# Performance work log

Measured on AMD Instinct MI355X. Metric: run time of the kernel, lower is better.

The kernel has to match this reference:

```python
import jax, jax.numpy as jnp
import numpy as np

D_MODEL = 1024
N_HEAD = 16
HEAD_DIM = D_MODEL // N_HEAD  # 64
B, T = 2, 2048
ROPE_BASE = 10000.0


def _rotary_cos_sin(seq_len, head_dim, dtype):
    inv_freq = 1.0 / (ROPE_BASE ** (jnp.arange(0, head_dim, 2, dtype=jnp.float32) / head_dim))
    t = jnp.arange(seq_len, dtype=jnp.float32)
    freqs = jnp.outer(t, inv_freq)  # [T, head_dim//2]
    cos = jnp.cos(freqs).astype(dtype)[None, :, None, :]  # [1,T,1,hd/2]
    sin = jnp.sin(freqs).astype(dtype)[None, :, None, :]
    return cos, sin


def _apply_rotary(x, cos, sin):
    d = x.shape[3] // 2
    x1, x2 = x[..., :d], x[..., d:]
    y1 = x1 * cos + x2 * sin
    y2 = -x1 * sin + x2 * cos
    return jnp.concatenate([y1, y2], axis=3).astype(x.dtype)


def setup_inputs() -> dict:
    key = jax.random.key(0)
    ks = jax.random.split(key, 7)
    s = 1.0 / np.sqrt(D_MODEL)
    return {
        "x": jax.random.normal(ks[0], (B, T, D_MODEL), dtype=jnp.float32),
        "Wq": jax.random.normal(ks[1], (D_MODEL, D_MODEL), dtype=jnp.float32) * s,
        "Wk": jax.random.normal(ks[2], (D_MODEL, D_MODEL), dtype=jnp.float32) * s,
        "Wq2": jax.random.normal(ks[3], (D_MODEL, D_MODEL), dtype=jnp.float32) * s,
        "Wk2": jax.random.normal(ks[4], (D_MODEL, D_MODEL), dtype=jnp.float32) * s,
        "Wv": jax.random.normal(ks[5], (D_MODEL, D_MODEL), dtype=jnp.float32) * s,
        "Wproj": jax.random.normal(ks[6], (D_MODEL, D_MODEL), dtype=jnp.float32) * s,
    }


def reference(x, Wq, Wk, Wq2, Wk2, Wv, Wproj):
    Bx, Tx, C = x.shape
    H, Dh = N_HEAD, HEAD_DIM

    def proj(W):
        return (x @ W.T).reshape(Bx, Tx, H, Dh)  # [B,T,H,Dh]

    q, k, q2, k2, v = proj(Wq), proj(Wk), proj(Wq2), proj(Wk2), proj(Wv)

    cos, sin = _rotary_cos_sin(Tx, Dh, x.dtype)
    q = _apply_rotary(q, cos, sin)
    k = _apply_rotary(k, cos, sin)
    q2 = _apply_rotary(q2, cos, sin)
    k2 = _apply_rotary(k2, cos, sin)

    scores = jnp.einsum('bqhd,bkhd->bhqk', q, k)
    scores2 = jnp.einsum('bqhd,bkhd->bhqk', q2, k2)
    pattern = (scores / Dh) * (scores2 / Dh)  # bilinear, no softmax
    causal = jnp.tril(jnp.ones((Tx, Tx), dtype=bool))
    pattern = jnp.where(causal[None, None, :, :], pattern, 0.0)

    z = jnp.einsum('bhqk,bkhd->bhqd', pattern, v)  # [B,H,T,Dh]
    y = z.transpose(0, 2, 1, 3).reshape(Bx, Tx, C)
    return y @ Wproj.T
```

## Files before the change

kernel.cpp:

```cpp
#include <hip/hip_runtime.h>
#include <hip/hip_bf16.h>

#define TSEQ 2048
#define NHEAD 16
#define DM 1024
#define NBATCH 2
#define MTOK (NBATCH * TSEQ)

typedef __attribute__((ext_vector_type(8))) short short8;
typedef __attribute__((ext_vector_type(4))) float floatx4;
typedef __attribute__((address_space(1))) const void gvoid;
typedef __attribute__((address_space(3))) void lvoid;

static __device__ __forceinline__ unsigned short f2bf(float f) {
    unsigned int u = __float_as_uint(f);
    return (unsigned short)((u + 0x7fffu + ((u >> 16) & 1u)) >> 16);
}
static __device__ __forceinline__ float bf2f(unsigned short h) {
    return __uint_as_float(((unsigned int)h) << 16);
}

__global__ __launch_bounds__(256)
void pack_all_kernel(const float* __restrict__ x,
                     const float* __restrict__ w0, const float* __restrict__ w1,
                     const float* __restrict__ w2, const float* __restrict__ w3,
                     const float* __restrict__ w4, const float* __restrict__ w5,
                     unsigned short* __restrict__ dstX, unsigned short* __restrict__ dstW)
{
    const float* src;
    unsigned short* dst;
    int gid;
    bool wlo = false, ilv = false;
    if (blockIdx.x < 4096) {
        src = x; dst = dstX;
        gid = blockIdx.x * 256 + threadIdx.x;
    } else {
        int wi = (blockIdx.x - 4096) >> 10;
        const float* srcs[6] = {w0, w1, w2, w3, w4, w5};
        src = srcs[wi];
        dst = dstW + (size_t)wi * 1024 * 2048;
        gid = ((blockIdx.x - 4096) & 1023) * 256 + threadIdx.x;
        wlo = (wi == 0);
        ilv = (wi >= 1 && wi <= 4);
    }
    int e   = gid * 4;
    int row = e >> 10;
    int col = e & 1023;
    float4 f = *(const float4*)(src + (size_t)row * 1024 + col);
    ushort4 hi, lo;
    hi.x = f2bf(f.x); lo.x = f2bf(f.x - bf2f(hi.x));
    hi.y = f2bf(f.y); lo.y = f2bf(f.y - bf2f(hi.y));
    hi.z = f2bf(f.z); lo.z = f2bf(f.z - bf2f(hi.z));
    hi.w = f2bf(f.w); lo.w = f2bf(f.w - bf2f(hi.w));
    int drow = row;
    if (ilv) {
        int hh = row >> 6, d = row & 63;
        int dd = (d < 32) ? ((d >> 3) * 16 + (d & 7))
                          : (((d - 32) >> 3) * 16 + 8 + (d & 7));
        drow = hh * 64 + dd;
    }
    *(ushort4*)(dst + (size_t)drow * 2048 + col) = hi;
    if (wlo)
        *(ushort4*)(dst + (size_t)drow * 2048 + 1024 + col) = lo;
}

#define VMW(N) asm volatile("s_waitcnt vmcnt(" #N ")" ::: "memory")
#define LGKM0  asm volatile("s_waitcnt lgkmcnt(0)" ::: "memory")

__global__ __launch_bounds__(512, 2)
void gemm_qkv(const unsigned short* __restrict__ Ap,
              const unsigned short* __restrict__ Bp,
              unsigned short* __restrict__ Ch, unsigned short* __restrict__ Vt)
{
    __shared__ __align__(16) unsigned short A0s[2][8192];
    __shared__ __align__(16) unsigned short A1s[2][8192];
    __shared__ __align__(16) unsigned short B0s[2][10240];
    __shared__ __align__(16) unsigned short B1s[2][10240];

    const int t    = threadIdx.x;
    const int lane = t & 63;
    const int w    = t >> 6;
    const int wm   = w >> 2;
    const int wn   = w & 3;
    const int s    = lane & 15;
    const int g    = (lane >> 4) & 3;
    const int row0 = blockIdx.x * 256;
    const int col0 = blockIdx.y * 320;

    const int cofs  = ((g ^ ((lane >> 1) & 3)) << 3);
    const int addrA = (wm * 128 + s) * 32 + cofs;
    const int addrB = (wn * 80 + s) * 32 + cofs;

    const int alc = (t & 3) ^ ((t >> 3) & 3);
    const unsigned short* Ag = Ap + (size_t)(row0 + (t >> 2)) * 2048 + alc * 8;
    const unsigned short* Bg = Bp + (size_t)(col0 + (t >> 2)) * 2048 + alc * 8;

#define STAGE_A(dst, kofs) {                                                                              \
    __builtin_amdgcn_global_load_lds((gvoid*)(Ag + (kofs)),              (lvoid*)((dst) + t * 8),        16, 0, 0); \
    __builtin_amdgcn_global_load_lds((gvoid*)(Ag + (kofs) + 128 * 2048), (lvoid*)((dst) + 4096 + t * 8), 16, 0, 0); }

#define STAGE_B(dst, kofs) {                                                                              \
    __builtin_amdgcn_global_load_lds((gvoid*)(Bg + (kofs)),              (lvoid*)((dst) + t * 8),        16, 0, 0); \
    __builtin_amdgcn_global_load_lds((gvoid*)(Bg + (kofs) + 128 * 2048), (lvoid*)((dst) + 4096 + t * 8), 16, 0, 0); \
    if (t < 256)                                                                                          \
    __builtin_amdgcn_global_load_lds((gvoid*)(Bg + (kofs) + 256 * 2048), (lvoid*)((dst) + 8192 + t * 8), 16, 0, 0); }

    floatx4 acc[8][5];
    #pragma unroll
    for (int ii = 0; ii < 8; ++ii)
        #pragma unroll
        for (int nf = 0; nf < 5; ++nf)
            acc[ii][nf] = (floatx4)(0.0f);

    STAGE_A(A0s[0], 0);
    STAGE_B(B0s[0], 0);
    STAGE_A(A1s[0], 32);
    STAGE_B(B1s[0], 32);
    STAGE_A(A0s[1], 64);
    STAGE_B(B0s[1], 64);
    VMW(4);
    __builtin_amdgcn_s_barrier();
    __builtin_amdgcn_sched_barrier(0);

#define MFMA_CLUSTER(IOFS)                                                                      \
    __builtin_amdgcn_s_setprio(1);                                                              \
    _Pragma("unroll")                                                                           \
    for (int ii = 0; ii < 4; ++ii)                                                              \
        _Pragma("unroll")                                                                       \
        for (int nf = 0; nf < 5; ++nf)                                                          \
            acc[(IOFS) + ii][nf] = __builtin_amdgcn_mfma_f32_16x16x32_bf16(af[ii], bf[nf], acc[(IOFS) + ii][nf], 0, 0, 0); \
    __builtin_amdgcn_s_setprio(0);

#define TILE_BODY(TAU, DO12, DO34, W2, W4)                                                      \
{                                                                                               \
    const int cur_ = (TAU) & 1;                                                                 \
    const unsigned short* a0k = A0s[cur_];                                                      \
    const unsigned short* a1k = A1s[cur_];                                                      \
    const unsigned short* b0k = B0s[cur_];                                                      \
    const unsigned short* b1k = B1s[cur_];                                                      \
    short8 af[4], bf[5];                                                                        \
                             \
    _Pragma("unroll")                                                                           \
    for (int ii = 0; ii < 4; ++ii) af[ii] = *(const short8*)&a0k[addrA + ii * 512];             \
    _Pragma("unroll")                                                                           \
    for (int nf = 0; nf < 5; ++nf) bf[nf] = *(const short8*)&b0k[addrB + nf * 512];             \
    if (DO12) STAGE_A(A1s[cur_ ^ 1], ((TAU) + 1) * 64 + 32);                                    \
    LGKM0;                                                                                      \
    __builtin_amdgcn_s_barrier();                                                               \
    __builtin_amdgcn_sched_barrier(0);                                                          \
    MFMA_CLUSTER(0)                                                                             \
                                  \
    _Pragma("unroll")                                                                           \
    for (int ii = 0; ii < 4; ++ii) af[ii] = *(const short8*)&a0k[addrA + (ii + 4) * 512];       \
    if (DO12) STAGE_B(B1s[cur_ ^ 1], ((TAU) + 1) * 64 + 32);                                    \
    LGKM0;                                                                                      \
    W2;                                                                                         \
    __builtin_amdgcn_s_barrier();                                                               \
    __builtin_amdgcn_sched_barrier(0);                                                          \
    MFMA_CLUSTER(4)                                                                             \
                             \
    _Pragma("unroll")                                                                           \
    for (int ii = 0; ii < 4; ++ii) af[ii] = *(const short8*)&a1k[addrA + ii * 512];             \
    _Pragma("unroll")                                                                           \
    for (int nf = 0; nf < 5; ++nf) bf[nf] = *(const short8*)&b1k[addrB + nf * 512];             \
    if (DO34) STAGE_A(A0s[cur_], ((TAU) + 2) * 64);                                             \
    LGKM0;                                                                                      \
    __builtin_amdgcn_s_barrier();                                                               \
    __builtin_amdgcn_sched_barrier(0);                                                          \
    MFMA_CLUSTER(0)                                                                             \
                                  \
    _Pragma("unroll")                                                                           \
    for (int ii = 0; ii < 4; ++ii) af[ii] = *(const short8*)&a1k[addrA + (ii + 4) * 512];       \
    if (DO34) STAGE_B(B0s[cur_], ((TAU) + 2) * 64);                                             \
    LGKM0;                                                                                      \
    W4;                                                                                        \
    __builtin_amdgcn_s_barrier();                                                               \
    __builtin_amdgcn_sched_barrier(0);                                                          \
    MFMA_CLUSTER(4)                                                                             \
}

    #pragma unroll 2
    for (int tau = 0; tau < 14; ++tau)
        TILE_BODY(tau, 1, 1, VMW(8), VMW(8));
    TILE_BODY(14, 1, 0, VMW(8), VMW(4));
    TILE_BODY(15, 0, 0, VMW(0), ((void)0));

#undef TILE_BODY
#undef MFMA_CLUSTER
#undef STAGE_A
#undef STAGE_B

    const int cr = (lane >> 4) * 4;
    const int cc = lane & 15;
    const int rwbase = row0 + wm * 128;
    const float L2C = -0.41524101186092029f;

    #pragma unroll
    for (int nf = 0; nf < 5; ++nf) {
        const int cg = col0 + wn * 80 + nf * 16;
        const int p  = cg >> 10;
        const int h  = (cg >> 6) & 15;
        const int f  = (cg >> 4) & 3;
        if (p < 4) {
            const float sc  = (p == 0 || p == 2) ? 0.015625f : 1.0f;
            const float inv = exp2f((float)(f * 8 + (cc & 7)) * L2C);
            unsigned short* hp = Ch + (size_t)p * 4194304;
            #pragma unroll
            for (int ii = 0; ii < 8; ++ii) {
                int r0  = rwbase + ii * 16 + cr;
                int bhi = ((r0 >> 11) << 4) + h;
                size_t base = ((size_t)bhi * 2048 + (r0 & 2047)) * 64;
                #pragma unroll
                for (int rr = 0; rr < 4; ++rr) {
                    float tt = (float)((r0 + rr) & 2047);
                    float s0, c0;
                    __sincosf(tt * inv, &s0, &c0);
                    float x  = acc[ii][nf][rr];
                    float xp = __shfl_xor(x, 8, 64);
                    float y  = (cc < 8) ? (x * c0 + xp * s0) : (x * c0 - xp * s0);
                    hp[base + (size_t)rr * 64 + (f * 16 + cc)] = f2bf(y * sc);
                }
            }
        } else {
            #pragma unroll
            for (int ii = 0; ii < 8; ++ii) {
                int r0  = rwbase + ii * 16 + cr;
                int bhi = ((r0 >> 11) << 4) + h;
                int d   = f * 16 + cc;
                ushort4 o;
                o.x = f2bf(acc[ii][nf][0]); o.y = f2bf(acc[ii][nf][1]);
                o.z = f2bf(acc[ii][nf][2]); o.w = f2bf(acc[ii][nf][3]);
                *(ushort4*)(Vt + ((size_t)bhi * 64 + d) * 2048 + (r0 & 2047)) = o;
            }
        }
    }
}

__global__ __launch_bounds__(256)
void gemm_proj(const unsigned short* __restrict__ Ap,
               const unsigned short* __restrict__ Bp,
               float* __restrict__ Cf)
{
    __shared__ __align__(16) unsigned short Ah[128 * 32];
    __shared__ __align__(16) unsigned short Al[128 * 32];
    __shared__ __align__(16) unsigned short Bh[128 * 32];
    __shared__ __align__(16) unsigned short Bl[128 * 32];

    const int t    = threadIdx.x;
    const int lane = t & 63;
    const int s    = lane & 15;
    const int row0 = blockIdx.x * 128;
    const int col0 = blockIdx.y * 128;
    const int m0   = ((t >> 6) >> 1) * 64;
    const int n0   = ((t >> 6) & 1) * 64;

    floatx4 acc[4][4];
    #pragma unroll
    for (int i = 0; i < 4; ++i)
        #pragma unroll
        for (int j = 0; j < 4; ++j)
            acc[i][j] = (floatx4)(0.0f);

    const int sr  = t >> 2;
    const int skx = ((t & 3) ^ ((t >> 3) & 3)) * 8;
    char* dA  = (char*)Ah + (size_t)t * 16;
    char* dAl = (char*)Al + (size_t)t * 16;
    char* dB  = (char*)Bh + (size_t)t * 16;
    char* dBl = (char*)Bl + (size_t)t * 16;
    const size_t arow = (size_t)(row0 + sr) * 2048 + skx;
    const size_t brow = (size_t)(col0 + sr) * 2048 + skx;

    #define ISSUE(k0)                                                                         \
    {                                                                                         \
        const unsigned short* ga = Ap + arow + (k0);                                          \
        const unsigned short* gb = Bp + brow + (k0);                                          \
        __builtin_amdgcn_global_load_lds((gvoid*)ga,                 (lvoid*)dA,          16, 0, 0); \
        __builtin_amdgcn_global_load_lds((gvoid*)(ga + 64*2048),     (lvoid*)(dA + 4096), 16, 0, 0); \
        __builtin_amdgcn_global_load_lds((gvoid*)(ga + 1024),        (lvoid*)dAl,         16, 0, 0); \
        __builtin_amdgcn_global_load_lds((gvoid*)(ga + 1024+64*2048),(lvoid*)(dAl + 4096),16, 0, 0); \
        __builtin_amdgcn_global_load_lds((gvoid*)gb,                 (lvoid*)dB,          16, 0, 0); \
        __builtin_amdgcn_global_load_lds((gvoid*)(gb + 64*2048),     (lvoid*)(dB + 4096), 16, 0, 0); \
        __builtin_amdgcn_global_load_lds((gvoid*)(gb + 1024),        (lvoid*)dBl,         16, 0, 0); \
        __builtin_amdgcn_global_load_lds((gvoid*)(gb + 1024+64*2048),(lvoid*)(dBl + 4096),16, 0, 0); \
    }

    const int cofs = (((lane >> 4) ^ ((lane >> 1) & 3)) << 3);

    ISSUE(0);
    for (int ks = 0; ks < 32; ++ks) {
        __syncthreads();
        short8 ahf[4], alf[4], bhf[4], blf[4];
        #pragma unroll
        for (int i = 0; i < 4; ++i) {
            int ra = (m0 + i * 16 + s) * 32 + cofs;
            ahf[i] = *(const short8*)&Ah[ra];
            alf[i] = *(const short8*)&Al[ra];
        }
        #pragma unroll
        for (int j = 0; j < 4; ++j) {
            int rb = (n0 + j * 16 + s) * 32 + cofs;
            bhf[j] = *(const short8*)&Bh[rb];
            blf[j] = *(const short8*)&Bl[rb];
        }
        #pragma unroll
        for (int i = 0; i < 4; ++i)
            #pragma unroll
            for (int j = 0; j < 4; ++j) {
                acc[i][j] = __builtin_amdgcn_mfma_f32_16x16x32_bf16(ahf[i], bhf[j], acc[i][j], 0, 0, 0);
                acc[i][j] = __builtin_amdgcn_mfma_f32_16x16x32_bf16(alf[i], bhf[j], acc[i][j], 0, 0, 0);
                acc[i][j] = __builtin_amdgcn_mfma_f32_16x16x32_bf16(ahf[i], blf[j], acc[i][j], 0, 0, 0);
            }
        __syncthreads();
        if (ks + 1 < 32) ISSUE((ks + 1) * 32);
    }
    #undef ISSUE

    const int cr = (lane >> 4) * 4;
    const int cc = lane & 15;
    #pragma unroll
    for (int i = 0; i < 4; ++i)
        #pragma unroll
        for (int j = 0; j < 4; ++j) {
            int r = row0 + m0 + i * 16 + cr;
            int c = col0 + n0 + j * 16 + cc;
            #pragma unroll
            for (int rr = 0; rr < 4; ++rr)
                Cf[(size_t)(r + rr) * 1024 + c] = acc[i][j][rr];
        }
}

__global__ __launch_bounds__(512, 2)
void attn_mfma(const unsigned short* __restrict__ qh, const unsigned short* __restrict__ q2h,
               const unsigned short* __restrict__ kh, const unsigned short* __restrict__ k2h,
               const unsigned short* __restrict__ vt, unsigned short* __restrict__ zout)
{
    __shared__ __align__(16) unsigned short smem[40960];
    unsigned short* qs  = smem;
    unsigned short* q2s = smem + 8192;
    unsigned short* psq = smem;
    unsigned short* ks  = smem + 16384;
    unsigned short* k2s = smem + 24576;
    unsigned short* vts = smem + 32768;

    const int bid  = blockIdx.x;
    const int xcd  = bid & 7;
    const int slot = bid >> 3;
    const int hh   = slot >> 3;
    const int pr   = slot & 7;
    const int bh   = xcd * 4 + hh;
    const int t  = threadIdx.x;
    const int lane = t & 63;
    const int w    = t >> 6;
    const int s    = lane & 15;
    const int g    = lane >> 4;
    const int mk   = (w >> 1) * 32;
    const int nq   = (w & 1) * 64;

    const int b = bh >> 4, h = bh & 15;

    short8 kf[2], k2f[2], vf[2];

#define LOADKV(TK) {                                                                \
    const unsigned short* kb  = kh  + ((size_t)bh * 2048 + (TK) * 128) * 64;        \
    const unsigned short* k2b = k2h + ((size_t)bh * 2048 + (TK) * 128) * 64;        \
    const unsigned short* vb  = vt  + (size_t)bh * 131072 + (TK) * 128;             \
    const int krow_ = t >> 2;                                                       \
    const int vd_   = t >> 3;                                                       \
    _Pragma("unroll")                                                               \
    for (int c = 0; c < 2; ++c) {                                                   \
        int cg_ = (t & 3) * 2 + c;                                                  \
        kf[c]  = *(const short8*)(kb  + (size_t)krow_ * 64 + cg_ * 8);              \
        k2f[c] = *(const short8*)(k2b + (size_t)krow_ * 64 + cg_ * 8);              \
        int cg16_ = (t & 7) * 2 + c;                                                \
        vf[c]  = *(const short8*)(vb + (size_t)vd_ * 2048 + cg16_ * 8);             \
    } }

    #pragma unroll
    for (int pass = 0; pass < 2; ++pass) {
        const int qt = pass ? pr : (15 - pr);

        __syncthreads();

        LOADKV(0);

        {
            const unsigned short* qb  = qh  + ((size_t)bh * 2048 + qt * 128) * 64;
            const unsigned short* q2b = q2h + ((size_t)bh * 2048 + qt * 128) * 64;
            const int row = t >> 2;
            #pragma unroll
            for (int c = 0; c < 2; ++c) {
                int cg  = (t & 3) * 2 + c;
                short8 a  = *(const short8*)(qb  + (size_t)row * 64 + cg * 8);
                short8 a2 = *(const short8*)(q2b + (size_t)row * 64 + cg * 8);
                int cgm = (cg + row) & 7;
                *(short8*)&qs [row * 64 + cgm * 8] = a;
                *(short8*)&q2s[row * 64 + cgm * 8] = a2;
            }
        }
        __syncthreads();
        short8 bq[2][4], bq2[2][4];
        #pragma unroll
        for (int kstep = 0; kstep < 2; ++kstep) {
            const int gl = kstep * 4 + g;
            #pragma unroll
            for (int j = 0; j < 4; ++j) {
                int row = nq + j * 16 + s;
                int a = row * 64 + ((gl + row) & 7) * 8;
                bq[kstep][j]  = *(const short8*)&qs [a];
                bq2[kstep][j] = *(const short8*)&q2s[a];
            }
        }

        floatx4 zac[4];
        #pragma unroll
        for (int j = 0; j < 4; ++j)
            zac[j] = (floatx4)(0.0f);

        for (int tk = 0; tk <= qt; ++tk) {
            __syncthreads();
            {
                const int krow = t >> 2;
                const int vd   = t >> 3;
                #pragma unroll
                for (int c = 0; c < 2; ++c) {
                    int cg  = (t & 3) * 2 + c;
                    int cgm = (cg + krow) & 7;
                    *(short8*)&ks [krow * 64 + cgm * 8] = kf[c];
                    *(short8*)&k2s[krow * 64 + cgm * 8] = k2f[c];
                    int cg16  = (t & 7) * 2 + c;
                    int cgm16 = (cg16 + vd) & 15;
                    *(short8*)&vts[vd * 128 + cgm16 * 8] = vf[c];
                }
            }
            __syncthreads();

            if (tk < qt) LOADKV(tk + 1);
            __builtin_amdgcn_sched_barrier(0);

            #pragma unroll
            for (int i = 0; i < 2; ++i) {
                floatx4 a1[4], a2[4];
                #pragma unroll
                for (int j = 0; j < 4; ++j) { a1[j] = (floatx4)(0.0f); a2[j] = (floatx4)(0.0f); }
                #pragma unroll
                for (int kstep = 0; kstep < 2; ++kstep) {
                    const int gl = kstep * 4 + g;
                    int row = mk + i * 16 + s;
                    int a = row * 64 + ((gl + row) & 7) * 8;
                    short8 ak  = *(const short8*)&ks [a];
                    short8 ak2 = *(const short8*)&k2s[a];
                    #pragma unroll
                    for (int j = 0; j < 4; ++j) {
                        a1[j] = __builtin_amdgcn_mfma_f32_16x16x32_bf16(ak,  bq[kstep][j],  a1[j], 0, 0, 0);
                        a2[j] = __builtin_amdgcn_mfma_f32_16x16x32_bf16(ak2, bq2[kstep][j], a2[j], 0, 0, 0);
                    }
                }
                const int kl0   = mk + i * 16 + g * 4;
                const int chunk = kl0 >> 3;
                const int sub   = kl0 & 7;
                if (tk < qt) {
                    #pragma unroll
                    for (int j = 0; j < 4; ++j) {
                        const int ql = nq + j * 16 + s;
                        ushort4 pw;
                        pw.x = f2bf(a1[j][0] * a2[j][0]);
                        pw.y = f2bf(a1[j][1] * a2[j][1]);
                        pw.z = f2bf(a1[j][2] * a2[j][2]);
                        pw.w = f2bf(a1[j][3] * a2[j][3]);
                        *(ushort4*)&psq[ql * 128 + ((chunk + ql) & 15) * 8 + sub] = pw;
                    }
                } else {
                    #pragma unroll
                    for (int j = 0; j < 4; ++j) {
                        const int ql = nq + j * 16 + s;
                        ushort4 pw;
                        pw.x = (kl0 + 0 <= ql) ? f2bf(a1[j][0] * a2[j][0]) : (unsigned short)0;
                        pw.y = (kl0 + 1 <= ql) ? f2bf(a1[j][1] * a2[j][1]) : (unsigned short)0;
                        pw.z = (kl0 + 2 <= ql) ? f2bf(a1[j][2] * a2[j][2]) : (unsigned short)0;
                        pw.w = (kl0 + 3 <= ql) ? f2bf(a1[j][3] * a2[j][3]) : (unsigned short)0;
                        *(ushort4*)&psq[ql * 128 + ((chunk + ql) & 15) * 8 + sub] = pw;
                    }
                }
            }

            __syncthreads();

            const int wm0 = w * 16;
            #pragma unroll
            for (int kstep = 0; kstep < 4; ++kstep) {
                const int cbase = kstep * 4 + g;
                short8 ap, bv[4];
                {
                    int q = wm0 + s;
                    ap = *(const short8*)&psq[q * 128 + ((cbase + q) & 15) * 8];
                }
                #pragma unroll
                for (int jd = 0; jd < 4; ++jd) {
                    int d = jd * 16 + s;
                    bv[jd] = *(const short8*)&vts[d * 128 + ((cbase + d) & 15) * 8];
                }
                #pragma unroll
                for (int jd = 0; jd < 4; ++jd)
                    zac[jd] = __builtin_amdgcn_mfma_f32_16x16x32_bf16(ap, bv[jd], zac[jd], 0, 0, 0);
            }
        }

        const size_t zrow0 = (size_t)(b * TSEQ + qt * 128);
        #pragma unroll
        for (int j = 0; j < 4; ++j)
            #pragma unroll
            for (int r = 0; r < 4; ++r) {
                float zv = zac[j][r];
                unsigned short hi = f2bf(zv);
                unsigned short lo = f2bf(zv - bf2f(hi));
                size_t row = zrow0 + w * 16 + g * 4 + r;
                int col = h * 64 + j * 16 + s;
                zout[row * 2048 + col]        = hi;
                zout[row * 2048 + 1024 + col] = lo;
            }
    }
#undef LOADKV
}

extern "C" void kernel_launch(void* const* d_in, const int* in_sizes, int n_in,
                              void* d_out, int out_size, void* d_ws, size_t ws_size,
                              hipStream_t stream)
{
    const float* x     = (const float*)d_in[0];
    const float* Wq    = (const float*)d_in[1];
    const float* Wk    = (const float*)d_in[2];
    const float* Wq2   = (const float*)d_in[3];
    const float* Wk2   = (const float*)d_in[4];
    const float* Wv    = (const float*)d_in[5];
    const float* Wproj = (const float*)d_in[6];

    unsigned short* Xp    = (unsigned short*)d_ws;
    unsigned short* Wp    = (unsigned short*)((char*)d_ws + 16777216);
    unsigned short* heads = (unsigned short*)((char*)d_ws + 41943040);
    unsigned short* vt    = (unsigned short*)((char*)d_ws + 75497472);

    const size_t HS = (size_t)32 * 2048 * 64;
    unsigned short* qh  = heads;
    unsigned short* kh  = heads + 1 * HS;
    unsigned short* q2h = heads + 2 * HS;
    unsigned short* k2h = heads + 3 * HS;

    pack_all_kernel<<<10240, 256, 0, stream>>>(x, Wproj, Wq, Wk, Wq2, Wk2, Wv, Xp, Wp);
    gemm_qkv<<<dim3(16, 16), 512, 0, stream>>>(Xp, Wp + (size_t)1024 * 2048, heads, vt);
    attn_mfma<<<256, 512, 0, stream>>>(qh, q2h, kh, k2h, vt, Xp);
    gemm_proj<<<dim3(32, 8), 256, 0, stream>>>(Xp, Wp, (float*)d_out);
}
```

Measured before the change: 228.8 us.

## Double-buffer K/K2/V tiles in LDS for the attention kernel

Splits the K, K2 and V shared-memory tiles into two alternating buffers. The next tile is written to LDS at the start of each iteration, and the global load for the tile two steps ahead is issued before the PV MFMA phase. This removes one barrier per iteration and overlaps staging with compute. LDS per block grows from 80KB to 128KB, so two 512-thread blocks may no longer fit on a CU, which would cut occupancy.

Result: no change. 227.9 us (-0.4%).

```diff
diff --git a/kernel.cpp b/kernel.cpp
--- a/kernel.cpp
+++ b/kernel.cpp
@@ -334,13 +334,11 @@
                const unsigned short* __restrict__ kh, const unsigned short* __restrict__ k2h,
                const unsigned short* __restrict__ vt, unsigned short* __restrict__ zout)
 {
-    __shared__ __align__(16) unsigned short smem[40960];
+    __shared__ __align__(16) unsigned short smem[65536];
     unsigned short* qs  = smem;
     unsigned short* q2s = smem + 8192;
     unsigned short* psq = smem;
-    unsigned short* ks  = smem + 16384;
-    unsigned short* k2s = smem + 24576;
-    unsigned short* vts = smem + 32768;
+    unsigned short* kvb = smem + 16384;
 
     const int bid  = blockIdx.x;
     const int xcd  = bid & 7;
@@ -375,6 +373,23 @@
         vf[c]  = *(const short8*)(vb + (size_t)vd_ * 2048 + cg16_ * 8);             \
     } }
 
+#define WRITEKV(DST) {                                                              \
+    unsigned short* ksd_  = (DST);                                                  \
+    unsigned short* k2sd_ = (DST) + 8192;                                           \
+    unsigned short* vtsd_ = (DST) + 16384;                                          \
+    const int krow_ = t >> 2;                                                       \
+    const int vd_   = t >> 3;                                                       \
+    _Pragma("unroll")                                                               \
+    for (int c = 0; c < 2; ++c) {                                                   \
+        int cg_  = (t & 3) * 2 + c;                                                 \
+        int cgm_ = (cg_ + krow_) & 7;                                               \
+        *(short8*)&ksd_ [krow_ * 64 + cgm_ * 8] = kf[c];                            \
+        *(short8*)&k2sd_[krow_ * 64 + cgm_ * 8] = k2f[c];                           \
+        int cg16_  = (t & 7) * 2 + c;                                               \
+        int cgm16_ = (cg16_ + vd_) & 15;                                            \
+        *(short8*)&vtsd_[vd_ * 128 + cgm16_ * 8] = vf[c];                           \
+    } }
+
     #pragma unroll
     for (int pass = 0; pass < 2; ++pass) {
         const int qt = pass ? pr : (15 - pr);
@@ -411,31 +426,21 @@
             }
         }
 
+        WRITEKV(kvb);
+        if (qt > 0) LOADKV(1);
+        __syncthreads();
+
         floatx4 zac[4];
         #pragma unroll
         for (int j = 0; j < 4; ++j)
             zac[j] = (floatx4)(0.0f);
 
         for (int tk = 0; tk <= qt; ++tk) {
-            __syncthreads();
-            {
-                const int krow = t >> 2;
-                const int vd   = t >> 3;
-                #pragma unroll
-                for (int c = 0; c < 2; ++c) {
-                    int cg  = (t & 3) * 2 + c;
-                    int cgm = (cg + krow) & 7;
-                    *(short8*)&ks [krow * 64 + cgm * 8] = kf[c];
-                    *(short8*)&k2s[krow * 64 + cgm * 8] = k2f[c];
-                    int cg16  = (t & 7) * 2 + c;
-                    int cgm16 = (cg16 + vd) & 15;
-                    *(short8*)&vts[vd * 128 + cgm16 * 8] = vf[c];
-                }
-            }
-            __syncthreads();
-
-            if (tk < qt) LOADKV(tk + 1);
-            __builtin_amdgcn_sched_barrier(0);
+            const int cur = tk & 1;
+            unsigned short* kvc = kvb + cur * 24576;
+            unsigned short* kvn = kvb + (cur ^ 1) * 24576;
+
+            if (tk < qt) WRITEKV(kvn);
 
             #pragma unroll
             for (int i = 0; i < 2; ++i) {
@@ -447,8 +452,8 @@
                     const int gl = kstep * 4 + g;
                     int row = mk + i * 16 + s;
                     int a = row * 64 + ((gl + row) & 7) * 8;
-                    short8 ak  = *(const short8*)&ks [a];
-                    short8 ak2 = *(const short8*)&k2s[a];
+                    short8 ak  = *(const short8*)&kvc[a];
+                    short8 ak2 = *(const short8*)&kvc[8192 + a];
                     #pragma unroll
                     for (int j = 0; j < 4; ++j) {
                         a1[j] = __builtin_amdgcn_mfma_f32_16x16x32_bf16(ak,  bq[kstep][j],  a1[j], 0, 0, 0);
@@ -485,6 +490,9 @@
 
             __syncthreads();
 
+            if (tk + 2 <= qt) LOADKV(tk + 2);
+            __builtin_amdgcn_sched_barrier(0);
+
             const int wm0 = w * 16;
             #pragma unroll
             for (int kstep = 0; kstep < 4; ++kstep) {
@@ -497,12 +505,14 @@
                 #pragma unroll
                 for (int jd = 0; jd < 4; ++jd) {
                     int d = jd * 16 + s;
-                    bv[jd] = *(const short8*)&vts[d * 128 + ((cbase + d) & 15) * 8];
+                    bv[jd] = *(const short8*)&kvc[16384 + d * 128 + ((cbase + d) & 15) * 8];
                 }
                 #pragma unroll
                 for (int jd = 0; jd < 4; ++jd)
                     zac[jd] = __builtin_amdgcn_mfma_f32_16x16x32_bf16(ap, bv[jd], zac[jd], 0, 0, 0);
             }
+
+            __syncthreads();
         }
 
         const size_t zrow0 = (size_t)(b * TSEQ + qt * 128);
@@ -520,6 +530,7 @@
             }
     }
 #undef LOADKV
+#undef WRITEKV
 }
 
 extern "C" void kernel_launch(void* const* d_in, const int* in_sizes, int n_in,
```
